# Kernel tuning notes

Measured on AMD Instinct MI355X. Metric: run time of the kernel, lower is better.

## Reference

```python
import jax, jax.numpy as jnp
import numpy as np

N = 100_000   # nodes
E = 3_200_000 # edges
K = 3         # num_stacks
T = 4         # num_layers (shared weights)
H = 16        # hidden channels of conv1
EPS = 1e-5    # BatchNorm eps


def setup_inputs() -> dict:
    key = jax.random.key(0)
    ks = jax.random.split(key, 12)
    def glorot(k, shape):
        fan = shape[-2] + shape[-1]
        return jax.random.normal(k, shape, jnp.float32) * (2.0 / fan) ** 0.5
    return {
        "x": jax.random.normal(ks[0], (N, 1), jnp.float32),
        "edge_index": jax.random.randint(ks[1], (2, E), 0, N, jnp.int32),
        "edge_weight": jax.random.uniform(ks[2], (E,), jnp.float32),
        # conv1: in=1, out=16  (init_weight [K,Fin,Fout], shared weight [K,Fout,Fout], root [K,Fin,Fout], bias [K,Fout])
        "conv1_init_w": glorot(ks[3], (K, 1, H)),
        "conv1_w": glorot(ks[4], (K, H, H)),
        "conv1_root_w": glorot(ks[5], (K, 1, H)),
        "conv1_bias": jnp.zeros((K, H), jnp.float32),
        # BatchNorm1d(16) in eval mode: running stats + affine params
        "bn1_gamma": jnp.ones((H,), jnp.float32),
        "bn1_beta": jnp.zeros((H,), jnp.float32),
        "bn1_mean": jnp.zeros((H,), jnp.float32),
        "bn1_var": jnp.ones((H,), jnp.float32),
        # conv2: in=16, out=1, act=None
        "conv2_init_w": glorot(ks[6], (K, H, 1)),
        "conv2_w": glorot(ks[7], (K, 1, 1)),
        "conv2_root_w": glorot(ks[8], (K, H, 1)),
        "conv2_bias": jnp.zeros((K, 1), jnp.float32),
    }


def _gcn_norm(edge_index, edge_weight):
    # ARMAConv uses gcn_norm with add_self_loops=False
    row, col = edge_index[0], edge_index[1]
    deg = jax.ops.segment_sum(edge_weight, col, num_segments=N)
    dis = jnp.where(deg > 0, jax.lax.rsqrt(jnp.maximum(deg, 1e-12)), 0.0)
    norm = dis[row] * edge_weight * dis[col]
    return row, col, norm


def _arma(x, row, col, norm, init_w, w, root_w, bias, act):
    # x: [N, Fin]; out per stack: [K, N, Fout]
    root = jnp.einsum('nf,kfo->kno', x, root_w) + bias[:, None, :]
    out = jnp.einsum('nf,kfo->kno', x, init_w)
    for t in range(T):
        if t > 0:
            out = jnp.einsum('kno,kop->knp', out, w)  # shared weight
        msg = out[:, row, :] * norm[None, :, None]     # [K, E, F] gather + scale
        out = jax.ops.segment_sum(msg.transpose(1, 0, 2), col, num_segments=N)  # [N, K, F]
        out = out.transpose(1, 0, 2) + root            # scatter-add + skip (root)
        if act:
            out = jax.nn.relu(out)
    return out.mean(axis=0)  # mean over stacks -> [N, Fout]


def reference(x, edge_index, edge_weight,
              conv1_init_w, conv1_w, conv1_root_w, conv1_bias,
              bn1_gamma, bn1_beta, bn1_mean, bn1_var,
              conv2_init_w, conv2_w, conv2_root_w, conv2_bias):
    row, col, norm = _gcn_norm(edge_index, edge_weight)
    h = _arma(x, row, col, norm, conv1_init_w, conv1_w, conv1_root_w, conv1_bias, act=True)
    # BatchNorm1d (eval) + ReLU; dropout is identity in eval
    h = (h - bn1_mean) * jax.lax.rsqrt(bn1_var + EPS) * bn1_gamma + bn1_beta
    h = jax.nn.relu(h)
    h = _arma(h, row, col, norm, conv2_init_w, conv2_w, conv2_root_w, conv2_bias, act=False)
    return jax.nn.sigmoid(h)  # [N, 1]
```

## Files before the change

kernel.cpp:

```cpp
#include <hip/hip_runtime.h>
#include <math.h>

#define NN 100000
#define NE 3200000
#define NB 782
#define EPB 4096
#define NBLK 782
#define BN_EPS 1e-5f

static inline size_t alignup(size_t v) { return (v + 255) & ~size_t(255); }

__device__ inline unsigned short f2bf(float x) {
  unsigned u = __float_as_uint(x);
  u += 0x7FFF + ((u >> 16) & 1);
  return (unsigned short)(u >> 16);
}
__device__ inline float bf2f(unsigned short h) {
  return __uint_as_float((unsigned)h << 16);
}

__global__ void k_hist(const int* __restrict__ col, int* __restrict__ cntm) {
  __shared__ int cnt[NB];
  for (int i = threadIdx.x; i < NB; i += 256) cnt[i] = 0;
  __syncthreads();
  int e0 = blockIdx.x * EPB;
  int nE = min(EPB, NE - e0);
  for (int i = threadIdx.x; i < nE; i += 256) atomicAdd(&cnt[col[e0 + i] >> 7], 1);
  __syncthreads();
  int* dst = cntm + (size_t)blockIdx.x * NB;
  for (int i = threadIdx.x; i < NB; i += 256) dst[i] = cnt[i];
}

__global__ void k_scanb(const int* __restrict__ cntm, int* __restrict__ basemT,
                        int* __restrict__ btot) {
  __shared__ int s[NBLK];
  __shared__ int c[256];
  const int NCH = (NBLK + 3) / 4;
  int q = blockIdx.x, t = threadIdx.x;
  for (int i = t; i < NBLK; i += 256) s[i] = cntm[(size_t)i * NB + q];
  __syncthreads();
  if (t < NCH) {
    int b0 = 4 * t, sum = 0;
    #pragma unroll
    for (int j = 0; j < 4; ++j) if (b0 + j < NBLK) sum += s[b0 + j];
    c[t] = sum;
  }
  __syncthreads();
  for (int d = 1; d < NCH; d <<= 1) {
    int v = (t < NCH && t >= d) ? c[t - d] : 0;
    __syncthreads();
    if (t < NCH) c[t] += v;
    __syncthreads();
  }
  if (t < NCH) {
    int b0 = 4 * t;
    int run = (t > 0) ? c[t - 1] : 0;
    #pragma unroll
    for (int j = 0; j < 4; ++j)
      if (b0 + j < NBLK) { int v = s[b0 + j]; s[b0 + j] = run; run += v; }
  }
  __syncthreads();
  int* dst = basemT + (size_t)q * NBLK;
  for (int i = t; i < NBLK; i += 256) dst[i] = s[i];
  if (t == 0) btot[q] = c[NCH - 1];
}

__global__ void k_scanq(const int* __restrict__ btot, int* __restrict__ gbase) {
  __shared__ int s[NB];
  __shared__ int c[256];
  const int NCH = (NB + 3) / 4;
  int t = threadIdx.x;
  for (int i = t; i < NB; i += 256) s[i] = btot[i];
  __syncthreads();
  if (t < NCH) {
    int b0 = 4 * t, sum = 0;
    #pragma unroll
    for (int j = 0; j < 4; ++j) if (b0 + j < NB) sum += s[b0 + j];
    c[t] = sum;
  }
  __syncthreads();
  for (int d = 1; d < NCH; d <<= 1) {
    int v = (t < NCH && t >= d) ? c[t - d] : 0;
    __syncthreads();
    if (t < NCH) c[t] += v;
    __syncthreads();
  }
  if (t < NCH) {
    int b0 = 4 * t;
    int run = (t > 0) ? c[t - 1] : 0;
    #pragma unroll
    for (int j = 0; j < 4; ++j)
      if (b0 + j < NB) { int v = s[b0 + j]; s[b0 + j] = run; run += v; }
  }
  __syncthreads();
  for (int i = t; i < NB; i += 256) gbase[i] = s[i];
}

__global__ void k_scat(const int* __restrict__ row, const int* __restrict__ col,
                       const float* __restrict__ ew, const int* __restrict__ basemT,
                       const int* __restrict__ gbase, int2* __restrict__ bin) {
  __shared__ int baseL[NB];
  __shared__ int cnt[NB];
  int b = blockIdx.x, t = threadIdx.x;
  for (int i = t; i < NB; i += 256) {
    baseL[i] = gbase[i] + basemT[(size_t)i * NBLK + b];
    cnt[i] = 0;
  }
  __syncthreads();
  int e0 = b * EPB;
  int nE = min(EPB, NE - e0);
  for (int i = t; i < nE; i += 256) {
    int e = e0 + i;
    int cc = col[e], q = cc >> 7;
    int r = atomicAdd(&cnt[q], 1);
    bin[baseL[q] + r] = make_int2(row[e] | ((cc & 127) << 17), __float_as_int(ew[e]));
  }
}

__global__ void k_build(const int* __restrict__ gbase, const int* __restrict__ btot,
                        const int2* __restrict__ bin,
                        int* __restrict__ csr, float* __restrict__ dis,
                        int* __restrict__ nstart, int* __restrict__ ncnt) {
  __shared__ int cnt[128];
  __shared__ float degw[128];
  __shared__ int off[129];
  int b = blockIdx.x;
  int gb0 = gbase[b];
  int nb = btot[b];
  const int2* gb = bin + gb0;
  for (int i = threadIdx.x; i < 128; i += 256) { cnt[i] = 0; degw[i] = 0.f; }
  __syncthreads();
  for (int i = threadIdx.x; i < nb; i += 256) {
    int2 v = gb[i];
    int c = (v.x >> 17) & 127;
    atomicAdd(&cnt[c], 1);
    atomicAdd(&degw[c], __int_as_float(v.y));
  }
  __syncthreads();
  if (threadIdx.x == 0) {
    int s = 0;
    for (int c = 0; c < 128; ++c) { off[c] = s; s += cnt[c]; }
    off[128] = s;
  }
  __syncthreads();
  for (int c = threadIdx.x; c < 128; c += 256) {
    int n = b * 128 + c;
    if (n < NN) {
      nstart[n] = gb0 + off[c];
      ncnt[n] = cnt[c];
      float d = degw[c];
      dis[n] = (d > 0.f) ? rsqrtf(fmaxf(d, 1e-12f)) : 0.f;
    }
  }
  __syncthreads();
  for (int i = threadIdx.x; i < 128; i += 256) cnt[i] = 0;
  __syncthreads();
  int* cb = csr + gb0;
  for (int i = threadIdx.x; i < nb; i += 256) {
    int2 v = gb[i];
    int c = (v.x >> 17) & 127;
    int pos = off[c] + atomicAdd(&cnt[c], 1);
    float w = __int_as_float(v.y);
    int q = (int)fminf(fmaf(w, 32767.f, 0.5f), 32767.f);
    cb[pos] = (v.x & 0x1FFFF) | (q << 17);
  }
}

__global__ void k_init1(const float* __restrict__ x, const float* __restrict__ rw,
                        const float* __restrict__ bias, const float* __restrict__ dis,
                        float* __restrict__ root1, float* __restrict__ s) {
  int idx = blockIdx.x * 256 + threadIdx.x;
  if (idx >= NN * 16) return;
  int n = idx >> 4, f = idx & 15;
  float xv = x[n];
  if (f == 0) s[n] = dis[n] * xv;
  root1[n * 48 + f]      = xv * rw[f]      + bias[f];
  root1[n * 48 + 16 + f] = xv * rw[16 + f] + bias[16 + f];
  root1[n * 48 + 32 + f] = xv * rw[32 + f] + bias[32 + f];
}

__global__ void k_prop_first(const float* __restrict__ s, const float* __restrict__ root,
                             ushort4* __restrict__ outp, const int* __restrict__ csr,
                             const int* __restrict__ nstart, const int* __restrict__ ncnt,
                             const float* __restrict__ dis, const float* __restrict__ w,
                             const float* __restrict__ iw) {
  __shared__ float ws[768];
  for (int i = threadIdx.x; i < 768; i += 256) ws[i] = w[i];
  __syncthreads();
  int f = threadIdx.x & 15;
  int n = (blockIdx.x * 256 + threadIdx.x) >> 4;
  if (n >= NN) return;
  int e0 = nstart[n], cnt = ncnt[n];
  float g = 0.f;
  for (int i = f; i < cnt; i += 16) {
    int e = csr[e0 + i];
    float we = (float)((unsigned)e >> 17) * (1.f / 32767.f);
    g = fmaf(we, s[e & 0x1FFFF], g);
  }
  #pragma unroll
  for (int d = 8; d; d >>= 1) g += __shfl_xor(g, d, 16);
  float dn = dis[n];
  float dg = dn * g;
  float a0 = fmaxf(fmaf(dg, iw[f],      root[n * 48 + f]),      0.f);
  float a1 = fmaxf(fmaf(dg, iw[16 + f], root[n * 48 + 16 + f]), 0.f);
  float a2 = fmaxf(fmaf(dg, iw[32 + f], root[n * 48 + 32 + f]), 0.f);
  float n0 = 0.f, n1 = 0.f, n2 = 0.f;
  #pragma unroll
  for (int f2 = 0; f2 < 16; ++f2) {
    float b0 = __shfl(a0, f2, 16);
    float b1 = __shfl(a1, f2, 16);
    float b2v = __shfl(a2, f2, 16);
    n0 = fmaf(b0, ws[f2 * 16 + f], n0);
    n1 = fmaf(b1, ws[256 + f2 * 16 + f], n1);
    n2 = fmaf(b2v, ws[512 + f2 * 16 + f], n2);
  }
  ushort4 pk;
  pk.x = f2bf(dn * n0); pk.y = f2bf(dn * n1); pk.z = f2bf(dn * n2); pk.w = 0;
  outp[(size_t)n * 16 + f] = pk;
}

template <bool APPLY_W>
__global__ void k_prop16(const ushort4* __restrict__ in, const float* __restrict__ root,
                         ushort4* __restrict__ outp, const int* __restrict__ csr,
                         const int* __restrict__ nstart, const int* __restrict__ ncnt,
                         const float* __restrict__ dis, const float* __restrict__ w,
                         const float* __restrict__ bng, const float* __restrict__ bnb,
                         const float* __restrict__ bnm, const float* __restrict__ bnv,
                         const float* __restrict__ iw2, const float* __restrict__ rw2,
                         const float* __restrict__ b2,
                         float4* __restrict__ root2, float4* __restrict__ o2) {
  __shared__ float ws[768];
  if (APPLY_W) {
    for (int i = threadIdx.x; i < 768; i += 256) ws[i] = w[i];
    __syncthreads();
  }
  int f = threadIdx.x & 15;
  int n = (blockIdx.x * 256 + threadIdx.x) >> 4;
  if (n >= NN) return;
  int e0 = nstart[n], cnt = ncnt[n];
  float a0 = 0.f, a1 = 0.f, a2 = 0.f;
  int i = 0;
  for (; i + 8 <= cnt; i += 8) {
    int e[8];
    ushort4 v[8];
    #pragma unroll
    for (int j = 0; j < 8; ++j) e[j] = csr[e0 + i + j];
    #pragma unroll
    for (int j = 0; j < 8; ++j) v[j] = in[(size_t)(e[j] & 0x1FFFF) * 16 + f];
    #pragma unroll
    for (int j = 0; j < 8; ++j) {
      float we = (float)((unsigned)e[j] >> 17) * (1.f / 32767.f);
      a0 = fmaf(we, bf2f(v[j].x), a0);
      a1 = fmaf(we, bf2f(v[j].y), a1);
      a2 = fmaf(we, bf2f(v[j].z), a2);
    }
  }
  for (; i + 4 <= cnt; i += 4) {
    int e[4];
    ushort4 v[4];
    #pragma unroll
    for (int j = 0; j < 4; ++j) e[j] = csr[e0 + i + j];
    #pragma unroll
    for (int j = 0; j < 4; ++j) v[j] = in[(size_t)(e[j] & 0x1FFFF) * 16 + f];
    #pragma unroll
    for (int j = 0; j < 4; ++j) {
      float we = (float)((unsigned)e[j] >> 17) * (1.f / 32767.f);
      a0 = fmaf(we, bf2f(v[j].x), a0);
      a1 = fmaf(we, bf2f(v[j].y), a1);
      a2 = fmaf(we, bf2f(v[j].z), a2);
    }
  }
  for (; i < cnt; ++i) {
    int e = csr[e0 + i];
    float we = (float)((unsigned)e >> 17) * (1.f / 32767.f);
    ushort4 v = in[(size_t)(e & 0x1FFFF) * 16 + f];
    a0 = fmaf(we, bf2f(v.x), a0);
    a1 = fmaf(we, bf2f(v.y), a1);
    a2 = fmaf(we, bf2f(v.z), a2);
  }
  float dn = dis[n];
  a0 = fmaxf(fmaf(dn, a0, root[n * 48 + f]), 0.f);
  a1 = fmaxf(fmaf(dn, a1, root[n * 48 + 16 + f]), 0.f);
  a2 = fmaxf(fmaf(dn, a2, root[n * 48 + 32 + f]), 0.f);
  if (APPLY_W) {
    float n0 = 0.f, n1 = 0.f, n2 = 0.f;
    #pragma unroll
    for (int f2 = 0; f2 < 16; ++f2) {
      float b0 = __shfl(a0, f2, 16);
      float b1 = __shfl(a1, f2, 16);
      float b2v = __shfl(a2, f2, 16);
      n0 = fmaf(b0, ws[f2 * 16 + f], n0);
      n1 = fmaf(b1, ws[256 + f2 * 16 + f], n1);
      n2 = fmaf(b2v, ws[512 + f2 * 16 + f], n2);
    }
    ushort4 pk;
    pk.x = f2bf(dn * n0); pk.y = f2bf(dn * n1); pk.z = f2bf(dn * n2); pk.w = 0;
    outp[(size_t)n * 16 + f] = pk;
  } else {
    float mean = (a0 + a1 + a2) * (1.f / 3.f);
    float hv = fmaxf((mean - bnm[f]) * rsqrtf(bnv[f] + BN_EPS) * bng[f] + bnb[f], 0.f);
    float d0 = hv * iw2[f],      r0 = hv * rw2[f];
    float d1 = hv * iw2[16 + f], r1 = hv * rw2[16 + f];
    float d2 = hv * iw2[32 + f], r2 = hv * rw2[32 + f];
    #pragma unroll
    for (int d = 8; d; d >>= 1) {
      d0 += __shfl_xor(d0, d, 16); r0 += __shfl_xor(r0, d, 16);
      d1 += __shfl_xor(d1, d, 16); r1 += __shfl_xor(r1, d, 16);
      d2 += __shfl_xor(d2, d, 16); r2 += __shfl_xor(r2, d, 16);
    }
    if (f == 0) {
      float4 rt, oo;
      rt.x = r0 + b2[0]; rt.y = r1 + b2[1]; rt.z = r2 + b2[2]; rt.w = 0.f;
      oo.x = dn * d0; oo.y = dn * d1; oo.z = dn * d2; oo.w = 0.f;
      root2[n] = rt;
      o2[n] = oo;
    }
  }
}

template <bool LAST>
__global__ void k_prop1(const float4* __restrict__ in, const float4* __restrict__ root,
                        float4* __restrict__ outp, float* __restrict__ outf,
                        const int* __restrict__ csr,
                        const int* __restrict__ nstart, const int* __restrict__ ncnt,
                        const float* __restrict__ dis, const float* __restrict__ w2) {
  int lane = threadIdx.x & 15;
  int n = (blockIdx.x * 256 + threadIdx.x) >> 4;
  if (n >= NN) return;
  int e0 = nstart[n], cnt = ncnt[n];
  float a0 = 0.f, a1 = 0.f, a2 = 0.f;
  for (int i = lane; i < cnt; i += 16) {
    int e = csr[e0 + i];
    float we = (float)((unsigned)e >> 17) * (1.f / 32767.f);
    float4 src = in[e & 0x1FFFF];
    a0 = fmaf(we, src.x, a0);
    a1 = fmaf(we, src.y, a1);
    a2 = fmaf(we, src.z, a2);
  }
  #pragma unroll
  for (int d = 8; d; d >>= 1) {
    a0 += __shfl_xor(a0, d, 16);
    a1 += __shfl_xor(a1, d, 16);
    a2 += __shfl_xor(a2, d, 16);
  }
  if (lane == 0) {
    float dn = dis[n];
    float4 rt = root[n];
    if (LAST) {
      float s = fmaf(dn, a0, rt.x) + fmaf(dn, a1, rt.y) + fmaf(dn, a2, rt.z);
      s *= (1.f / 3.f);
      outf[n] = 1.f / (1.f + expf(-s));
    } else {
      float4 oo;
      oo.x = dn * fmaf(dn, a0, rt.x) * w2[0];
      oo.y = dn * fmaf(dn, a1, rt.y) * w2[1];
      oo.z = dn * fmaf(dn, a2, rt.z) * w2[2];
      oo.w = 0.f;
      outp[n] = oo;
    }
  }
}

extern "C" void kernel_launch(void* const* d_in, const int* in_sizes, int n_in,
                              void* d_out, int out_size, void* d_ws, size_t ws_size,
                              hipStream_t stream) {
  const float* x     = (const float*)d_in[0];
  const int*   ei    = (const int*)d_in[1];
  const float* ew    = (const float*)d_in[2];
  const float* c1_iw = (const float*)d_in[3];
  const float* c1_w  = (const float*)d_in[4];
  const float* c1_rw = (const float*)d_in[5];
  const float* c1_b  = (const float*)d_in[6];
  const float* bn_g  = (const float*)d_in[7];
  const float* bn_b  = (const float*)d_in[8];
  const float* bn_m  = (const float*)d_in[9];
  const float* bn_v  = (const float*)d_in[10];
  const float* c2_iw = (const float*)d_in[11];
  const float* c2_w  = (const float*)d_in[12];
  const float* c2_rw = (const float*)d_in[13];
  const float* c2_b  = (const float*)d_in[14];
  float* out = (float*)d_out;

  char* p = (char*)d_ws;
  auto take = [&](size_t bytes) -> char* { char* r = p; p += alignup(bytes); return r; };
  int*     cntm   = (int*)take((size_t)NBLK * NB * 4);
  int*     basemT = (int*)take((size_t)NB * NBLK * 4);
  int*     btot   = (int*)take((size_t)NB * 4);
  int*     gbase  = (int*)take((size_t)NB * 4);
  int2*    bin    = (int2*)take((size_t)NE * 8);
  int*     csr    = (int*)take((size_t)NE * 4);
  float*   dis    = (float*)take((size_t)NN * 4);
  int*     nst    = (int*)take((size_t)NN * 4);
  int*     ncn    = (int*)take((size_t)NN * 4);
  float*   root1  = (float*)take((size_t)NN * 48 * 4);
  float*   sbuf   = (float*)take((size_t)NN * 4);
  ushort4* bufA   = (ushort4*)take((size_t)NN * 16 * 8);
  ushort4* bufB   = (ushort4*)take((size_t)NN * 16 * 8);
  float4*  root2  = (float4*)take((size_t)NN * 16);
  float4*  o2A    = (float4*)take((size_t)NN * 16);
  float4*  o2B    = (float4*)take((size_t)NN * 16);

  const int* row = ei;
  const int* col = ei + NE;

  const int gP = (NN * 16 + 255) / 256;

  k_hist <<<NBLK, 256, 0, stream>>>(col, cntm);
  k_scanb<<<NB, 256, 0, stream>>>(cntm, basemT, btot);
  k_scanq<<<1, 256, 0, stream>>>(btot, gbase);
  k_scat <<<NBLK, 256, 0, stream>>>(row, col, ew, basemT, gbase, bin);
  k_build<<<NB, 256, 0, stream>>>(gbase, btot, bin, csr, dis, nst, ncn);

  k_init1<<<gP, 256, 0, stream>>>(x, c1_rw, c1_b, dis, root1, sbuf);
  k_prop_first<<<gP, 256, 0, stream>>>(sbuf, root1, bufA, csr, nst, ncn, dis, c1_w, c1_iw);
  k_prop16<true ><<<gP, 256, 0, stream>>>(bufA, root1, bufB, csr, nst, ncn, dis, c1_w,
      nullptr, nullptr, nullptr, nullptr, nullptr, nullptr, nullptr, nullptr, nullptr);
  k_prop16<true ><<<gP, 256, 0, stream>>>(bufB, root1, bufA, csr, nst, ncn, dis, c1_w,
      nullptr, nullptr, nullptr, nullptr, nullptr, nullptr, nullptr, nullptr, nullptr);
  k_prop16<false><<<gP, 256, 0, stream>>>(bufA, root1, nullptr, csr, nst, ncn, dis, nullptr,
      bn_g, bn_b, bn_m, bn_v, c2_iw, c2_rw, c2_b, root2, o2A);

  k_prop1<false><<<gP, 256, 0, stream>>>(o2A, root2, o2B, nullptr, csr, nst, ncn, dis, c2_w);
  k_prop1<false><<<gP, 256, 0, stream>>>(o2B, root2, o2A, nullptr, csr, nst, ncn, dis, c2_w);
  k_prop1<false><<<gP, 256, 0, stream>>>(o2A, root2, o2B, nullptr, csr, nst, ncn, dis, c2_w);
  k_prop1<true ><<<gP, 256, 0, stream>>>(o2B, root2, nullptr, out, csr, nst, ncn, dis, c2_w);
}
```

Baseline: 386.6 us.

## Coarsen CSR buckets, stage scatter in LDS, and batch column scans

Each bucket now holds 256 destination nodes instead of 128, which halves the bucket count. The per-bucket column scan is replaced by a kernel that scans 16 buckets per block using wave shuffles and writes the bases in block-major layout. The scatter kernel now sorts each block's edges locally in LDS before writing them out, so global writes into each bucket segment are contiguous instead of random. This costs an extra local histogram pass, a local scan and about 40KB of LDS per block, which may reduce occupancy.

```diff
diff --git a/kernel.cpp b/kernel.cpp
--- a/kernel.cpp
+++ b/kernel.cpp
@@ -3,9 +3,10 @@
 
 #define NN 100000
 #define NE 3200000
-#define NB 782
+#define NBUCK 391
 #define EPB 4096
 #define NBLK 782
+#define SB_Q 16
 #define BN_EPS 1e-5f
 
 static inline size_t alignup(size_t v) { return (v + 255) & ~size_t(255); }
@@ -20,29 +21,63 @@
 }
 
 __global__ void k_hist(const int* __restrict__ col, int* __restrict__ cntm) {
-  __shared__ int cnt[NB];
-  for (int i = threadIdx.x; i < NB; i += 256) cnt[i] = 0;
+  __shared__ int cnt[NBUCK];
+  for (int i = threadIdx.x; i < NBUCK; i += 256) cnt[i] = 0;
   __syncthreads();
   int e0 = blockIdx.x * EPB;
   int nE = min(EPB, NE - e0);
-  for (int i = threadIdx.x; i < nE; i += 256) atomicAdd(&cnt[col[e0 + i] >> 7], 1);
-  __syncthreads();
-  int* dst = cntm + (size_t)blockIdx.x * NB;
-  for (int i = threadIdx.x; i < NB; i += 256) dst[i] = cnt[i];
-}
-
-__global__ void k_scanb(const int* __restrict__ cntm, int* __restrict__ basemT,
+  for (int i = threadIdx.x; i < nE; i += 256) atomicAdd(&cnt[col[e0 + i] >> 8], 1);
+  __syncthreads();
+  int* dst = cntm + (size_t)blockIdx.x * NBUCK;
+  for (int i = threadIdx.x; i < NBUCK; i += 256) dst[i] = cnt[i];
+}
+
+__global__ void k_scanb(const int* __restrict__ cntm, int* __restrict__ basem,
                         int* __restrict__ btot) {
-  __shared__ int s[NBLK];
+  __shared__ int s[NBLK][SB_Q + 1];
+  int q0 = blockIdx.x * SB_Q;
+  int nq = min(SB_Q, NBUCK - q0);
+  int t = threadIdx.x;
+  for (int idx = t; idx < NBLK * SB_Q; idx += 256) {
+    int i = idx >> 4, j = idx & 15;
+    s[i][j] = (j < nq) ? cntm[(size_t)i * NBUCK + q0 + j] : 0;
+  }
+  __syncthreads();
+  int wave = t >> 6, lane = t & 63;
+  for (int j = wave; j < SB_Q; j += 4) {
+    int carry = 0;
+    for (int c = 0; c < (NBLK + 63) / 64; ++c) {
+      int i = c * 64 + lane;
+      int v = (i < NBLK) ? s[i][j] : 0;
+      int x = v;
+      #pragma unroll
+      for (int d = 1; d < 64; d <<= 1) {
+        int tt = __shfl_up(x, d, 64);
+        if (lane >= d) x += tt;
+      }
+      if (i < NBLK) s[i][j] = x - v + carry;
+      carry += __shfl(x, 63, 64);
+    }
+    if (lane == 0 && j < nq) btot[q0 + j] = carry;
+  }
+  __syncthreads();
+  for (int idx = t; idx < NBLK * SB_Q; idx += 256) {
+    int i = idx >> 4, j = idx & 15;
+    if (j < nq) basem[(size_t)i * NBUCK + q0 + j] = s[i][j];
+  }
+}
+
+__global__ void k_scanq(const int* __restrict__ btot, int* __restrict__ gbase) {
+  __shared__ int s[NBUCK];
   __shared__ int c[256];
-  const int NCH = (NBLK + 3) / 4;
-  int q = blockIdx.x, t = threadIdx.x;
-  for (int i = t; i < NBLK; i += 256) s[i] = cntm[(size_t)i * NB + q];
+  const int NCH = (NBUCK + 3) / 4;
+  int t = threadIdx.x;
+  for (int i = t; i < NBUCK; i += 256) s[i] = btot[i];
   __syncthreads();
   if (t < NCH) {
     int b0 = 4 * t, sum = 0;
     #pragma unroll
-    for (int j = 0; j < 4; ++j) if (b0 + j < NBLK) sum += s[b0 + j];
+    for (int j = 0; j < 4; ++j) if (b0 + j < NBUCK) sum += s[b0 + j];
     c[t] = sum;
   }
   __syncthreads();
@@ -57,63 +92,68 @@
     int run = (t > 0) ? c[t - 1] : 0;
     #pragma unroll
     for (int j = 0; j < 4; ++j)
-      if (b0 + j < NBLK) { int v = s[b0 + j]; s[b0 + j] = run; run += v; }
-  }
-  __syncthreads();
-  int* dst = basemT + (size_t)q * NBLK;
-  for (int i = t; i < NBLK; i += 256) dst[i] = s[i];
-  if (t == 0) btot[q] = c[NCH - 1];
-}
-
-__global__ void k_scanq(const int* __restrict__ btot, int* __restrict__ gbase) {
-  __shared__ int s[NB];
-  __shared__ int c[256];
-  const int NCH = (NB + 3) / 4;
-  int t = threadIdx.x;
-  for (int i = t; i < NB; i += 256) s[i] = btot[i];
-  __syncthreads();
-  if (t < NCH) {
-    int b0 = 4 * t, sum = 0;
-    #pragma unroll
-    for (int j = 0; j < 4; ++j) if (b0 + j < NB) sum += s[b0 + j];
-    c[t] = sum;
-  }
-  __syncthreads();
-  for (int d = 1; d < NCH; d <<= 1) {
-    int v = (t < NCH && t >= d) ? c[t - d] : 0;
-    __syncthreads();
-    if (t < NCH) c[t] += v;
-    __syncthreads();
-  }
-  if (t < NCH) {
-    int b0 = 4 * t;
-    int run = (t > 0) ? c[t - 1] : 0;
-    #pragma unroll
-    for (int j = 0; j < 4; ++j)
-      if (b0 + j < NB) { int v = s[b0 + j]; s[b0 + j] = run; run += v; }
-  }
-  __syncthreads();
-  for (int i = t; i < NB; i += 256) gbase[i] = s[i];
+      if (b0 + j < NBUCK) { int v = s[b0 + j]; s[b0 + j] = run; run += v; }
+  }
+  __syncthreads();
+  for (int i = t; i < NBUCK; i += 256) gbase[i] = s[i];
 }
 
 __global__ void k_scat(const int* __restrict__ row, const int* __restrict__ col,
-                       const float* __restrict__ ew, const int* __restrict__ basemT,
+                       const float* __restrict__ ew, const int* __restrict__ basem,
                        const int* __restrict__ gbase, int2* __restrict__ bin) {
-  __shared__ int baseL[NB];
-  __shared__ int cnt[NB];
+  __shared__ int segB[NBUCK];
+  __shared__ int cnt[NBUCK];
+  __shared__ int csc[256];
+  __shared__ int2 stage[EPB];
+  __shared__ unsigned short qarr[EPB];
   int b = blockIdx.x, t = threadIdx.x;
-  for (int i = t; i < NB; i += 256) {
-    baseL[i] = gbase[i] + basemT[(size_t)i * NBLK + b];
+  for (int i = t; i < NBUCK; i += 256) {
+    segB[i] = gbase[i] + basem[(size_t)b * NBUCK + i];
     cnt[i] = 0;
   }
   __syncthreads();
   int e0 = b * EPB;
   int nE = min(EPB, NE - e0);
+  for (int i = t; i < nE; i += 256) atomicAdd(&cnt[col[e0 + i] >> 8], 1);
+  __syncthreads();
+  const int NCH = (NBUCK + 3) / 4;
+  int q4 = 4 * t;
+  if (t < NCH) {
+    int sum = 0;
+    #pragma unroll
+    for (int j = 0; j < 4; ++j) if (q4 + j < NBUCK) sum += cnt[q4 + j];
+    csc[t] = sum;
+  }
+  __syncthreads();
+  for (int d = 1; d < NCH; d <<= 1) {
+    int v = (t < NCH && t >= d) ? csc[t - d] : 0;
+    __syncthreads();
+    if (t < NCH) csc[t] += v;
+    __syncthreads();
+  }
+  if (t < NCH) {
+    int run = (t > 0) ? csc[t - 1] : 0;
+    #pragma unroll
+    for (int j = 0; j < 4; ++j)
+      if (q4 + j < NBUCK) {
+        int v = cnt[q4 + j];
+        segB[q4 + j] -= run;
+        cnt[q4 + j] = run;
+        run += v;
+      }
+  }
+  __syncthreads();
   for (int i = t; i < nE; i += 256) {
     int e = e0 + i;
-    int cc = col[e], q = cc >> 7;
-    int r = atomicAdd(&cnt[q], 1);
-    bin[baseL[q] + r] = make_int2(row[e] | ((cc & 127) << 17), __float_as_int(ew[e]));
+    int cc = col[e], q = cc >> 8;
+    int p = atomicAdd(&cnt[q], 1);
+    stage[p] = make_int2(row[e] | ((cc & 255) << 17), __float_as_int(ew[e]));
+    qarr[p] = (unsigned short)q;
+  }
+  __syncthreads();
+  for (int p = t; p < nE; p += 256) {
+    int q = qarr[p];
+    bin[segB[q] + p] = stage[p];
   }
 }
 
@@ -121,30 +161,30 @@
                         const int2* __restrict__ bin,
                         int* __restrict__ csr, float* __restrict__ dis,
                         int* __restrict__ nstart, int* __restrict__ ncnt) {
-  __shared__ int cnt[128];
-  __shared__ float degw[128];
-  __shared__ int off[129];
+  __shared__ int cnt[256];
+  __shared__ float degw[256];
+  __shared__ int off[257];
   int b = blockIdx.x;
   int gb0 = gbase[b];
   int nb = btot[b];
   const int2* gb = bin + gb0;
-  for (int i = threadIdx.x; i < 128; i += 256) { cnt[i] = 0; degw[i] = 0.f; }
+  for (int i = threadIdx.x; i < 256; i += 256) { cnt[i] = 0; degw[i] = 0.f; }
   __syncthreads();
   for (int i = threadIdx.x; i < nb; i += 256) {
     int2 v = gb[i];
-    int c = (v.x >> 17) & 127;
+    int c = (v.x >> 17) & 255;
     atomicAdd(&cnt[c], 1);
     atomicAdd(&degw[c], __int_as_float(v.y));
   }
   __syncthreads();
   if (threadIdx.x == 0) {
     int s = 0;
-    for (int c = 0; c < 128; ++c) { off[c] = s; s += cnt[c]; }
-    off[128] = s;
-  }
-  __syncthreads();
-  for (int c = threadIdx.x; c < 128; c += 256) {
-    int n = b * 128 + c;
+    for (int c = 0; c < 256; ++c) { off[c] = s; s += cnt[c]; }
+    off[256] = s;
+  }
+  __syncthreads();
+  for (int c = threadIdx.x; c < 256; c += 256) {
+    int n = b * 256 + c;
     if (n < NN) {
       nstart[n] = gb0 + off[c];
       ncnt[n] = cnt[c];
@@ -153,12 +193,12 @@
     }
   }
   __syncthreads();
-  for (int i = threadIdx.x; i < 128; i += 256) cnt[i] = 0;
+  for (int i = threadIdx.x; i < 256; i += 256) cnt[i] = 0;
   __syncthreads();
   int* cb = csr + gb0;
   for (int i = threadIdx.x; i < nb; i += 256) {
     int2 v = gb[i];
-    int c = (v.x >> 17) & 127;
+    int c = (v.x >> 17) & 255;
     int pos = off[c] + atomicAdd(&cnt[c], 1);
     float w = __int_as_float(v.y);
     int q = (int)fminf(fmaf(w, 32767.f, 0.5f), 32767.f);
@@ -383,10 +423,10 @@
 
   char* p = (char*)d_ws;
   auto take = [&](size_t bytes) -> char* { char* r = p; p += alignup(bytes); return r; };
-  int*     cntm   = (int*)take((size_t)NBLK * NB * 4);
-  int*     basemT = (int*)take((size_t)NB * NBLK * 4);
-  int*     btot   = (int*)take((size_t)NB * 4);
-  int*     gbase  = (int*)take((size_t)NB * 4);
+  int*     cntm   = (int*)take((size_t)NBLK * NBUCK * 4);
+  int*     basem  = (int*)take((size_t)NBLK * NBUCK * 4);
+  int*     btot   = (int*)take((size_t)NBUCK * 4);
+  int*     gbase  = (int*)take((size_t)NBUCK * 4);
   int2*    bin    = (int2*)take((size_t)NE * 8);
   int*     csr    = (int*)take((size_t)NE * 4);
   float*   dis    = (float*)take((size_t)NN * 4);
@@ -404,12 +444,13 @@
   const int* col = ei + NE;
 
   const int gP = (NN * 16 + 255) / 256;
+  const int gSB = (NBUCK + SB_Q - 1) / SB_Q;
 
   k_hist <<<NBLK, 256, 0, stream>>>(col, cntm);
-  k_scanb<<<NB, 256, 0, stream>>>(cntm, basemT, btot);
+  k_scanb<<<gSB, 256, 0, stream>>>(cntm, basem, btot);
   k_scanq<<<1, 256, 0, stream>>>(btot, gbase);
-  k_scat <<<NBLK, 256, 0, stream>>>(row, col, ew, basemT, gbase, bin);
-  k_build<<<NB, 256, 0, stream>>>(gbase, btot, bin, csr, dis, nst, ncn);
+  k_scat <<<NBLK, 256, 0, stream>>>(row, col, ew, basem, gbase, bin);
+  k_build<<<NBUCK, 256, 0, stream>>>(gbase, btot, bin, csr, dis, nst, ncn);
 
   k_init1<<<gP, 256, 0, stream>>>(x, c1_rw, c1_b, dis, root1, sbuf);
   k_prop_first<<<gP, 256, 0, stream>>>(sbuf, root1, bufA, csr, nst, ncn, dis, c1_w, c1_iw);
```

After: 398.6 us. 3.1% more time.
